# Optimization experiments

Hardware: AMD Instinct MI355X
Metric: run time of the kernel (lower is better)

Reference implementation:

```python
import jax, jax.numpy as jnp
import numpy as np
import math

B, SQ, SK, D = 32, 2048, 2048, 128


def setup_inputs() -> dict:
    key = jax.random.key(0)
    kq, kk, kv = jax.random.split(key, 3)
    queries = jax.random.normal(kq, (B, SQ, D), dtype=jnp.float32)
    keys = jax.random.normal(kk, (B, SK, D), dtype=jnp.float32)
    values = jax.random.normal(kv, (B, SK, D), dtype=jnp.float32)
    # causal mask: True = masked (future positions), broadcast over batch
    causal = jnp.triu(jnp.ones((SQ, SK), dtype=bool), k=1)
    mask = jnp.broadcast_to(causal, (B, SQ, SK))
    return {"queries": queries, "keys": keys, "values": values, "mask": mask}


def reference(queries, keys, values, mask):
    d = queries.shape[-1]
    scale = 1.0 / math.sqrt(d)
    # [B, Sq, Sk] score matrix (the module materializes this explicitly)
    scores = jnp.einsum("bqd,bkd->bqk", queries, keys) * scale
    scores = jnp.where(mask, -jnp.inf, scores)
    attn = jax.nn.softmax(scores, axis=-1)
    # dropout p=0.0 -> identity (eval parity)
    return jnp.einsum("bqk,bkd->bqd", attn, values)
```

## Files before the change

### kernel.cpp

```cpp
#include <hip/hip_runtime.h>
#include <hip/hip_bf16.h>

#define NB   32
#define SQL  2048
#define SKL  2048
#define DH   128
#define QBLK 128
#define KBLK 64

#define KSTR 136
#define VSTR 72
#define PSTR 72

typedef __attribute__((ext_vector_type(4))) float f32x4;
typedef __attribute__((ext_vector_type(8))) short s16x8;

__device__ __forceinline__ unsigned int pk2(float lo, float hi) {
  unsigned short a = __builtin_bit_cast(unsigned short, __float2bfloat16(lo));
  unsigned short b = __builtin_bit_cast(unsigned short, __float2bfloat16(hi));
  return (unsigned int)a | ((unsigned int)b << 16);
}

__global__ __launch_bounds__(512, 2)
void attn_fwd(const float* __restrict__ Qg, const float* __restrict__ Kg,
              const float* __restrict__ Vg, float* __restrict__ Og) {
  __shared__ __align__(16) unsigned short smem[2*64*KSTR + 2*128*VSTR + 8*16*PSTR];

  const int tid  = threadIdx.x;
  const int wid  = tid >> 6;
  const int lane = tid & 63;
  const int g    = lane >> 4;
  const int ln   = lane & 15;

  const int i    = blockIdx.x;
  const int half = i >> 8;
  const int idx  = i & 255;
  const int b    = idx >> 3;
  const int q3   = idx & 7;
  const int qt   = half ? q3 : (15 - q3);
  const int qb   = qt * QBLK;
  const int nt   = 2*qt + 2;

  const float* Qb = Qg + (size_t)b * SQL * DH;
  const float* Kb = Kg + (size_t)b * SKL * DH;
  const float* Vb = Vg + (size_t)b * SKL * DH;
  float* Ob = Og + (size_t)b * SQL * DH;

  const float qscale = 0.08838834764831845f * 1.4426950408889634f;

  s16x8 qf[4];
  {
    const float* qr = Qb + (size_t)(qb + 16*wid + ln) * DH + 8*g;
    #pragma unroll
    for (int c = 0; c < 4; ++c) {
      f32x4 a  = *(const f32x4*)(qr + 32*c);
      f32x4 b4 = *(const f32x4*)(qr + 32*c + 4);
      s16x8 q8;
      #pragma unroll
      for (int j = 0; j < 4; ++j) {
        q8[j]     = (short)(unsigned short)(pk2(a[j]  * qscale, 0.f) & 0xFFFF);
        q8[j + 4] = (short)(unsigned short)(pk2(b4[j] * qscale, 0.f) & 0xFFFF);
      }
      qf[c] = q8;
    }
  }

  f32x4 oacc[8];
  #pragma unroll
  for (int ot = 0; ot < 8; ++ot) oacc[ot] = (f32x4){0.f, 0.f, 0.f, 0.f};
  float m_run = -1e30f;
  float l_run = 0.f;

  const int qglob = qb + 16*wid + ln;
  const int qmax  = qb + 16*wid + 15;

  const int kcol  = tid & 31;
  const int krow0 = tid >> 5;
  const int vkq   = tid & 15;
  const int vdq   = tid >> 4;

  f32x4 kpre[4], vpre[4];

  {
    const float* ks = Kb;
    #pragma unroll
    for (int it = 0; it < 4; ++it)
      kpre[it] = *(const f32x4*)(ks + (size_t)(krow0 + 16*it) * DH + 4*kcol);
    const float* vs = Vb + 4*vdq;
    #pragma unroll
    for (int j = 0; j < 4; ++j)
      vpre[j] = *(const f32x4*)(vs + (size_t)(4*vkq + j) * DH);
  }

  for (int t = 0; t < nt; ++t) {
    const int buf = t & 1;
    const int kb  = t * KBLK;

    {
      unsigned short* Kl = smem + buf * (64*KSTR);
      #pragma unroll
      for (int it = 0; it < 4; ++it) {
        f32x4 v = kpre[it];
        uint2 pk = make_uint2(pk2(v[0], v[1]), pk2(v[2], v[3]));
        *(uint2*)&Kl[(krow0 + 16*it)*KSTR + 4*kcol] = pk;
      }
      unsigned short* Vl = smem + 2*(64*KSTR) + buf * (128*VSTR);
      #pragma unroll
      for (int j2 = 0; j2 < 4; ++j2) {
        uint2 pk = make_uint2(pk2(vpre[0][j2], vpre[1][j2]),
                              pk2(vpre[2][j2], vpre[3][j2]));
        *(uint2*)&Vl[(4*vdq + j2)*VSTR + 4*vkq] = pk;
      }
    }

    if (t + 1 < nt) {
      const int kn = (t + 1) * KBLK;
      const float* ks = Kb + (size_t)kn * DH;
      #pragma unroll
      for (int it = 0; it < 4; ++it)
        kpre[it] = *(const f32x4*)(ks + (size_t)(krow0 + 16*it) * DH + 4*kcol);
      const float* vs = Vb + (size_t)kn * DH + 4*vdq;
      #pragma unroll
      for (int j = 0; j < 4; ++j)
        vpre[j] = *(const f32x4*)(vs + (size_t)(4*vkq + j) * DH);
    }

    asm volatile("s_waitcnt lgkmcnt(0)" ::: "memory");
    __builtin_amdgcn_s_barrier();
    __builtin_amdgcn_sched_barrier(0);

    if (kb <= qmax) {
      const unsigned short* Kl = smem + buf * (64*KSTR);
      const unsigned short* Vl = smem + 2*(64*KSTR) + buf * (128*VSTR);
      unsigned short* Pl = smem + 2*(64*KSTR) + 2*(128*VSTR) + wid*(16*PSTR);

      f32x4 sacc[4];
      #pragma unroll
      for (int m = 0; m < 4; ++m) sacc[m] = (f32x4){0.f, 0.f, 0.f, 0.f};
      __builtin_amdgcn_s_setprio(1);
      #pragma unroll
      for (int c = 0; c < 4; ++c) {
        #pragma unroll
        for (int m = 0; m < 4; ++m) {
          s16x8 kf = *(const s16x8*)&Kl[(16*m + ln)*KSTR + 8*g + 32*c];
          sacc[m] = __builtin_amdgcn_mfma_f32_16x16x32_bf16(kf, qf[c], sacc[m], 0, 0, 0);
        }
      }
      __builtin_amdgcn_s_setprio(0);

      if (kb + KBLK - 1 > qb + 16*wid) {
        #pragma unroll
        for (int m = 0; m < 4; ++m)
          #pragma unroll
          for (int r = 0; r < 4; ++r) {
            const int kk = kb + 16*m + 4*g + r;
            if (kk > qglob) sacc[m][r] = -1e30f;
          }
      }

      float tmax = sacc[0][0];
      #pragma unroll
      for (int m = 0; m < 4; ++m)
        #pragma unroll
        for (int r = 0; r < 4; ++r) tmax = fmaxf(tmax, sacc[m][r]);
      tmax = fmaxf(tmax, __shfl_xor(tmax, 16));
      tmax = fmaxf(tmax, __shfl_xor(tmax, 32));
      const float mnew  = fmaxf(m_run, tmax);
      const float alpha = exp2f(m_run - mnew);
      float lsum = 0.f;
      unsigned int pw[4][2];
      #pragma unroll
      for (int m = 0; m < 4; ++m) {
        float p0 = exp2f(sacc[m][0] - mnew);
        float p1 = exp2f(sacc[m][1] - mnew);
        float p2 = exp2f(sacc[m][2] - mnew);
        float p3 = exp2f(sacc[m][3] - mnew);
        lsum += (p0 + p1) + (p2 + p3);
        pw[m][0] = pk2(p0, p1);
        pw[m][1] = pk2(p2, p3);
      }
      lsum += __shfl_xor(lsum, 16);
      lsum += __shfl_xor(lsum, 32);
      l_run = l_run * alpha + lsum;
      m_run = mnew;

      float ar[4];
      #pragma unroll
      for (int r = 0; r < 4; ++r) ar[r] = __shfl(alpha, 4*g + r);
      #pragma unroll
      for (int ot = 0; ot < 8; ++ot)
        #pragma unroll
        for (int r = 0; r < 4; ++r) oacc[ot][r] *= ar[r];

      {
        unsigned short* prow = Pl + ln*PSTR;
        #pragma unroll
        for (int m = 0; m < 4; ++m) {
          *(unsigned int*)&prow[16*m + 4*g]     = pw[m][0];
          *(unsigned int*)&prow[16*m + 4*g + 2] = pw[m][1];
        }
      }

      s16x8 pf[2];
      #pragma unroll
      for (int c2 = 0; c2 < 2; ++c2)
        pf[c2] = *(const s16x8*)&Pl[ln*PSTR + 8*g + 32*c2];
      __builtin_amdgcn_s_setprio(1);
      #pragma unroll
      for (int ot = 0; ot < 8; ++ot) {
        #pragma unroll
        for (int c2 = 0; c2 < 2; ++c2) {
          s16x8 vf = *(const s16x8*)&Vl[(16*ot + ln)*VSTR + 8*g + 32*c2];
          oacc[ot] = __builtin_amdgcn_mfma_f32_16x16x32_bf16(pf[c2], vf, oacc[ot], 0, 0, 0);
        }
      }
      __builtin_amdgcn_s_setprio(0);
    }
  }

  const float linv = 1.0f / l_run;
  float lr[4];
  #pragma unroll
  for (int r = 0; r < 4; ++r) lr[r] = __shfl(linv, 4*g + r);
  float* orow = Ob + (size_t)(qb + 16*wid) * DH + ln;
  #pragma unroll
  for (int ot = 0; ot < 8; ++ot)
    #pragma unroll
    for (int r = 0; r < 4; ++r)
      orow[(size_t)(4*g + r) * DH + 16*ot] = oacc[ot][r] * lr[r];
}

extern "C" void kernel_launch(void* const* d_in, const int* in_sizes, int n_in,
                              void* d_out, int out_size, void* d_ws, size_t ws_size,
                              hipStream_t stream) {
  const float* Q = (const float*)d_in[0];
  const float* K = (const float*)d_in[1];
  const float* V = (const float*)d_in[2];
  float* O = (float*)d_out;
  dim3 grid(NB * (SQL / QBLK));
  dim3 block(512);
  attn_fwd<<<grid, block, 0, stream>>>(Q, K, V, O);
}
```

Baseline: 103.6 us.

## Switch attention to 32x32 MFMA with 4 waves, swizzled LDS, register-resident P

Moves the kernel from 16x16x32 to 32x32x16 bf16 MFMA, with each of 4 waves now owning 32 query rows instead of 8 waves with 16 rows. The padded LDS strides are replaced by XOR-swizzled K/V tiles. P goes from registers into the PV MFMA through v_permlane32_swap rather than a round trip through LDS. The online softmax now skips the rescale unless the max grows by more than 8 (lazy rescaling), and packing uses v_cvt_pk_bf16. The aim is fewer LDS reads and writes, fewer instructions and fewer rescales per tile, at the cost of higher register pressure and fewer waves per block.

```diff
diff --git a/kernel.cpp b/kernel.cpp
--- a/kernel.cpp
+++ b/kernel.cpp
@@ -3,17 +3,21 @@
 
 #define NB   32
 #define SQL  2048
-#define SKL  2048
 #define DH   128
 #define QBLK 128
 #define KBLK 64
 
-#define KSTR 136
-#define VSTR 72
-#define PSTR 72
-
-typedef __attribute__((ext_vector_type(4))) float f32x4;
-typedef __attribute__((ext_vector_type(8))) short s16x8;
+typedef __attribute__((ext_vector_type(4)))  float f32x4;
+typedef __attribute__((ext_vector_type(16))) float f32x16;
+typedef __attribute__((ext_vector_type(8)))  short s16x8;
+typedef __attribute__((ext_vector_type(4)))  unsigned int u32x4;
+
+__device__ __forceinline__ unsigned int cvtpk_bf16(float lo, float hi) {
+  unsigned int r;
+  asm("v_cvt_pk_bf16_f32 %0, %1, %2" : "=v"(r) : "v"(lo), "v"(hi));
+  return r;
+}
+#define PLSWAP(x, y) asm volatile("v_permlane32_swap_b32 %0, %1" : "+v"(x), "+v"(y))
 
 __device__ __forceinline__ unsigned int pk2(float lo, float hi) {
   unsigned short a = __builtin_bit_cast(unsigned short, __float2bfloat16(lo));
@@ -21,16 +25,16 @@
   return (unsigned int)a | ((unsigned int)b << 16);
 }
 
-__global__ __launch_bounds__(512, 2)
+__global__ __launch_bounds__(256, 2)
 void attn_fwd(const float* __restrict__ Qg, const float* __restrict__ Kg,
               const float* __restrict__ Vg, float* __restrict__ Og) {
-  __shared__ __align__(16) unsigned short smem[2*64*KSTR + 2*128*VSTR + 8*16*PSTR];
+  __shared__ __align__(16) char smem[65536];
 
   const int tid  = threadIdx.x;
   const int wid  = tid >> 6;
   const int lane = tid & 63;
-  const int g    = lane >> 4;
-  const int ln   = lane & 15;
+  const int hi   = lane >> 5;
+  const int c    = lane & 31;
 
   const int i    = blockIdx.x;
   const int half = i >> 8;
@@ -39,195 +43,211 @@
   const int q3   = idx & 7;
   const int qt   = half ? q3 : (15 - q3);
   const int qb   = qt * QBLK;
-  const int nt   = 2*qt + 2;
+  const int nt   = 2 * qt + 2;
 
   const float* Qb = Qg + (size_t)b * SQL * DH;
-  const float* Kb = Kg + (size_t)b * SKL * DH;
-  const float* Vb = Vg + (size_t)b * SKL * DH;
+  const float* Kb = Kg + (size_t)b * SQL * DH;
+  const float* Vb = Vg + (size_t)b * SQL * DH;
   float* Ob = Og + (size_t)b * SQL * DH;
 
   const float qscale = 0.08838834764831845f * 1.4426950408889634f;
 
-  s16x8 qf[4];
+  s16x8 qf[8];
   {
-    const float* qr = Qb + (size_t)(qb + 16*wid + ln) * DH + 8*g;
-    #pragma unroll
-    for (int c = 0; c < 4; ++c) {
-      f32x4 a  = *(const f32x4*)(qr + 32*c);
-      f32x4 b4 = *(const f32x4*)(qr + 32*c + 4);
-      s16x8 q8;
-      #pragma unroll
-      for (int j = 0; j < 4; ++j) {
-        q8[j]     = (short)(unsigned short)(pk2(a[j]  * qscale, 0.f) & 0xFFFF);
-        q8[j + 4] = (short)(unsigned short)(pk2(b4[j] * qscale, 0.f) & 0xFFFF);
-      }
-      qf[c] = q8;
-    }
-  }
-
-  f32x4 oacc[8];
+    const float* qr = Qb + (size_t)(qb + 32*wid + c) * DH + 8*hi;
+    #pragma unroll
+    for (int ds = 0; ds < 8; ++ds) {
+      f32x4 a = *(const f32x4*)(qr + 16*ds);
+      f32x4 d = *(const f32x4*)(qr + 16*ds + 4);
+      u32x4 w;
+      w[0] = pk2(a[0]*qscale, a[1]*qscale);
+      w[1] = pk2(a[2]*qscale, a[3]*qscale);
+      w[2] = pk2(d[0]*qscale, d[1]*qscale);
+      w[3] = pk2(d[2]*qscale, d[3]*qscale);
+      qf[ds] = __builtin_bit_cast(s16x8, w);
+    }
+  }
+
+  f32x16 oacc[4];
   #pragma unroll
-  for (int ot = 0; ot < 8; ++ot) oacc[ot] = (f32x4){0.f, 0.f, 0.f, 0.f};
-  float m_run = -1e30f;
-  float l_run = 0.f;
-
-  const int qglob = qb + 16*wid + ln;
-  const int qmax  = qb + 16*wid + 15;
-
-  const int kcol  = tid & 31;
-  const int krow0 = tid >> 5;
-  const int vkq   = tid & 15;
-  const int vdq   = tid >> 4;
-
-  f32x4 kpre[4], vpre[4];
-
+  for (int nb = 0; nb < 4; ++nb) oacc[nb] = (f32x16){0.f};
+  float m_run = -1e30f, l_run = 0.f;
+
+  const int qglob = qb + 32*wid + c;
+  const int qhiw  = qb + 32*wid + 31;
+  const int qlow  = qb + 32*wid;
+
+  const int kr  = tid >> 4;
+  const int kc8 = tid & 15;
+  const int vkq = tid & 15;
+  const int vdq = tid >> 4;
+
+  f32x4 kpre[8], vpre[8];
   {
-    const float* ks = Kb;
-    #pragma unroll
-    for (int it = 0; it < 4; ++it)
-      kpre[it] = *(const f32x4*)(ks + (size_t)(krow0 + 16*it) * DH + 4*kcol);
-    const float* vs = Vb + 4*vdq;
-    #pragma unroll
-    for (int j = 0; j < 4; ++j)
-      vpre[j] = *(const f32x4*)(vs + (size_t)(4*vkq + j) * DH);
+    #pragma unroll
+    for (int it = 0; it < 4; ++it) {
+      const float* p = Kb + (size_t)(kr + 16*it) * DH + 8*kc8;
+      kpre[2*it]   = *(const f32x4*)(p);
+      kpre[2*it+1] = *(const f32x4*)(p + 4);
+    }
+    #pragma unroll
+    for (int dd = 0; dd < 2; ++dd)
+      #pragma unroll
+      for (int j = 0; j < 4; ++j)
+        vpre[4*dd + j] = *(const f32x4*)(Vb + (size_t)(4*vkq + j) * DH + 4*(vdq + 16*dd));
   }
 
   for (int t = 0; t < nt; ++t) {
     const int buf = t & 1;
     const int kb  = t * KBLK;
-
-    {
-      unsigned short* Kl = smem + buf * (64*KSTR);
-      #pragma unroll
-      for (int it = 0; it < 4; ++it) {
-        f32x4 v = kpre[it];
-        uint2 pk = make_uint2(pk2(v[0], v[1]), pk2(v[2], v[3]));
-        *(uint2*)&Kl[(krow0 + 16*it)*KSTR + 4*kcol] = pk;
-      }
-      unsigned short* Vl = smem + 2*(64*KSTR) + buf * (128*VSTR);
+    char* Kl = smem + buf * 16384;
+    char* Vl = smem + 32768 + buf * 16384;
+
+    #pragma unroll
+    for (int it = 0; it < 4; ++it) {
+      const int row = kr + 16*it;
+      f32x4 a = kpre[2*it], d2 = kpre[2*it+1];
+      u32x4 w;
+      w[0] = pk2(a[0], a[1]);  w[1] = pk2(a[2], a[3]);
+      w[2] = pk2(d2[0], d2[1]); w[3] = pk2(d2[2], d2[3]);
+      *(u32x4*)(Kl + ((row*256 + 16*kc8) ^ ((row & 7) << 4))) = w;
+    }
+    #pragma unroll
+    for (int dd = 0; dd < 2; ++dd)
       #pragma unroll
       for (int j2 = 0; j2 < 4; ++j2) {
-        uint2 pk = make_uint2(pk2(vpre[0][j2], vpre[1][j2]),
-                              pk2(vpre[2][j2], vpre[3][j2]));
-        *(uint2*)&Vl[(4*vdq + j2)*VSTR + 4*vkq] = pk;
-      }
-    }
+        const int row = 4*(vdq + 16*dd) + j2;
+        uint2 pkk = make_uint2(pk2(vpre[4*dd+0][j2], vpre[4*dd+1][j2]),
+                               pk2(vpre[4*dd+2][j2], vpre[4*dd+3][j2]));
+        *(uint2*)(Vl + ((row*128 + 8*vkq) ^ ((row & 7) << 4))) = pkk;
+      }
 
     if (t + 1 < nt) {
       const int kn = (t + 1) * KBLK;
       const float* ks = Kb + (size_t)kn * DH;
       #pragma unroll
-      for (int it = 0; it < 4; ++it)
-        kpre[it] = *(const f32x4*)(ks + (size_t)(krow0 + 16*it) * DH + 4*kcol);
-      const float* vs = Vb + (size_t)kn * DH + 4*vdq;
-      #pragma unroll
-      for (int j = 0; j < 4; ++j)
-        vpre[j] = *(const f32x4*)(vs + (size_t)(4*vkq + j) * DH);
+      for (int it = 0; it < 4; ++it) {
+        const float* p = ks + (size_t)(kr + 16*it) * DH + 8*kc8;
+        kpre[2*it]   = *(const f32x4*)(p);
+        kpre[2*it+1] = *(const f32x4*)(p + 4);
+      }
+      const float* vs = Vb + (size_t)kn * DH;
+      #pragma unroll
+      for (int dd = 0; dd < 2; ++dd)
+        #pragma unroll
+        for (int j = 0; j < 4; ++j)
+          vpre[4*dd + j] = *(const f32x4*)(vs + (size_t)(4*vkq + j) * DH + 4*(vdq + 16*dd));
     }
 
     asm volatile("s_waitcnt lgkmcnt(0)" ::: "memory");
     __builtin_amdgcn_s_barrier();
     __builtin_amdgcn_sched_barrier(0);
 
-    if (kb <= qmax) {
-      const unsigned short* Kl = smem + buf * (64*KSTR);
-      const unsigned short* Vl = smem + 2*(64*KSTR) + buf * (128*VSTR);
-      unsigned short* Pl = smem + 2*(64*KSTR) + 2*(128*VSTR) + wid*(16*PSTR);
-
-      f32x4 sacc[4];
-      #pragma unroll
-      for (int m = 0; m < 4; ++m) sacc[m] = (f32x4){0.f, 0.f, 0.f, 0.f};
+    if (kb <= qhiw) {
+      f32x16 sacc[2];
+      sacc[0] = (f32x16){0.f};
+      sacc[1] = (f32x16){0.f};
       __builtin_amdgcn_s_setprio(1);
       #pragma unroll
-      for (int c = 0; c < 4; ++c) {
-        #pragma unroll
-        for (int m = 0; m < 4; ++m) {
-          s16x8 kf = *(const s16x8*)&Kl[(16*m + ln)*KSTR + 8*g + 32*c];
-          sacc[m] = __builtin_amdgcn_mfma_f32_16x16x32_bf16(kf, qf[c], sacc[m], 0, 0, 0);
+      for (int ds = 0; ds < 8; ++ds) {
+        #pragma unroll
+        for (int mb = 0; mb < 2; ++mb) {
+          const int row = 32*mb + c;
+          s16x8 kf = *(const s16x8*)(Kl + ((row*256 + 32*ds + 16*hi) ^ ((c & 7) << 4)));
+          sacc[mb] = __builtin_amdgcn_mfma_f32_32x32x16_bf16(kf, qf[ds], sacc[mb], 0, 0, 0);
         }
       }
       __builtin_amdgcn_s_setprio(0);
 
-      if (kb + KBLK - 1 > qb + 16*wid) {
-        #pragma unroll
-        for (int m = 0; m < 4; ++m)
+      if (kb + KBLK - 1 > qlow) {
+        #pragma unroll
+        for (int mb = 0; mb < 2; ++mb)
           #pragma unroll
-          for (int r = 0; r < 4; ++r) {
-            const int kk = kb + 16*m + 4*g + r;
-            if (kk > qglob) sacc[m][r] = -1e30f;
+          for (int r = 0; r < 16; ++r) {
+            const int kk = kb + 32*mb + (r & 3) + 8*(r >> 2) + 4*hi;
+            if (kk > qglob) sacc[mb][r] = -1e30f;
           }
       }
 
-      float tmax = sacc[0][0];
-      #pragma unroll
-      for (int m = 0; m < 4; ++m)
-        #pragma unroll
-        for (int r = 0; r < 4; ++r) tmax = fmaxf(tmax, sacc[m][r]);
-      tmax = fmaxf(tmax, __shfl_xor(tmax, 16));
+      float mx[8];
+      #pragma unroll
+      for (int e = 0; e < 8; ++e)
+        mx[e] = fmaxf(fmaxf(sacc[0][e], sacc[0][e+8]), fmaxf(sacc[1][e], sacc[1][e+8]));
+      mx[0] = fmaxf(mx[0], mx[4]); mx[1] = fmaxf(mx[1], mx[5]);
+      mx[2] = fmaxf(mx[2], mx[6]); mx[3] = fmaxf(mx[3], mx[7]);
+      float tmax = fmaxf(fmaxf(mx[0], mx[1]), fmaxf(mx[2], mx[3]));
       tmax = fmaxf(tmax, __shfl_xor(tmax, 32));
-      const float mnew  = fmaxf(m_run, tmax);
-      const float alpha = exp2f(m_run - mnew);
+
+      if (!__all(tmax <= m_run + 8.0f)) {
+        const float mnew  = fmaxf(m_run, tmax);
+        const float alpha = exp2f(m_run - mnew);
+        #pragma unroll
+        for (int r = 0; r < 16; ++r) {
+          float av = __shfl(alpha, (r & 3) + 8*(r >> 2) + 4*hi);
+          #pragma unroll
+          for (int nb = 0; nb < 4; ++nb) oacc[nb][r] *= av;
+        }
+        l_run *= alpha;
+        m_run = mnew;
+      }
+
       float lsum = 0.f;
-      unsigned int pw[4][2];
-      #pragma unroll
-      for (int m = 0; m < 4; ++m) {
-        float p0 = exp2f(sacc[m][0] - mnew);
-        float p1 = exp2f(sacc[m][1] - mnew);
-        float p2 = exp2f(sacc[m][2] - mnew);
-        float p3 = exp2f(sacc[m][3] - mnew);
-        lsum += (p0 + p1) + (p2 + p3);
-        pw[m][0] = pk2(p0, p1);
-        pw[m][1] = pk2(p2, p3);
-      }
-      lsum += __shfl_xor(lsum, 16);
+      unsigned int u0[8], u1[8];
+      {
+        float p[16];
+        #pragma unroll
+        for (int r = 0; r < 16; ++r) p[r] = exp2f(sacc[0][r] - m_run);
+        lsum += ((p[0]+p[1])+(p[2]+p[3])) + ((p[4]+p[5])+(p[6]+p[7]))
+              + ((p[8]+p[9])+(p[10]+p[11])) + ((p[12]+p[13])+(p[14]+p[15]));
+        #pragma unroll
+        for (int w = 0; w < 8; ++w) u0[w] = cvtpk_bf16(p[2*w], p[2*w+1]);
+      }
+      {
+        float p[16];
+        #pragma unroll
+        for (int r = 0; r < 16; ++r) p[r] = exp2f(sacc[1][r] - m_run);
+        lsum += ((p[0]+p[1])+(p[2]+p[3])) + ((p[4]+p[5])+(p[6]+p[7]))
+              + ((p[8]+p[9])+(p[10]+p[11])) + ((p[12]+p[13])+(p[14]+p[15]));
+        #pragma unroll
+        for (int w = 0; w < 8; ++w) u1[w] = cvtpk_bf16(p[2*w], p[2*w+1]);
+      }
       lsum += __shfl_xor(lsum, 32);
-      l_run = l_run * alpha + lsum;
-      m_run = mnew;
-
-      float ar[4];
-      #pragma unroll
-      for (int r = 0; r < 4; ++r) ar[r] = __shfl(alpha, 4*g + r);
-      #pragma unroll
-      for (int ot = 0; ot < 8; ++ot)
-        #pragma unroll
-        for (int r = 0; r < 4; ++r) oacc[ot][r] *= ar[r];
-
-      {
-        unsigned short* prow = Pl + ln*PSTR;
-        #pragma unroll
-        for (int m = 0; m < 4; ++m) {
-          *(unsigned int*)&prow[16*m + 4*g]     = pw[m][0];
-          *(unsigned int*)&prow[16*m + 4*g + 2] = pw[m][1];
+      l_run += lsum;
+
+      PLSWAP(u0[0], u0[2]); PLSWAP(u0[1], u0[3]);
+      PLSWAP(u0[4], u0[6]); PLSWAP(u0[5], u0[7]);
+      PLSWAP(u1[0], u1[2]); PLSWAP(u1[1], u1[3]);
+      PLSWAP(u1[4], u1[6]); PLSWAP(u1[5], u1[7]);
+      s16x8 pa[4];
+      { u32x4 w = {u0[0], u0[1], u0[2], u0[3]}; pa[0] = __builtin_bit_cast(s16x8, w); }
+      { u32x4 w = {u0[4], u0[5], u0[6], u0[7]}; pa[1] = __builtin_bit_cast(s16x8, w); }
+      { u32x4 w = {u1[0], u1[1], u1[2], u1[3]}; pa[2] = __builtin_bit_cast(s16x8, w); }
+      { u32x4 w = {u1[4], u1[5], u1[6], u1[7]}; pa[3] = __builtin_bit_cast(s16x8, w); }
+
+      __builtin_amdgcn_s_setprio(1);
+      #pragma unroll
+      for (int nb = 0; nb < 4; ++nb) {
+        #pragma unroll
+        for (int ks = 0; ks < 4; ++ks) {
+          const int row = 32*nb + c;
+          s16x8 vf = *(const s16x8*)(Vl + ((row*128 + 32*ks + 16*hi) ^ ((c & 7) << 4)));
+          oacc[nb] = __builtin_amdgcn_mfma_f32_32x32x16_bf16(pa[ks], vf, oacc[nb], 0, 0, 0);
         }
       }
-
-      s16x8 pf[2];
-      #pragma unroll
-      for (int c2 = 0; c2 < 2; ++c2)
-        pf[c2] = *(const s16x8*)&Pl[ln*PSTR + 8*g + 32*c2];
-      __builtin_amdgcn_s_setprio(1);
-      #pragma unroll
-      for (int ot = 0; ot < 8; ++ot) {
-        #pragma unroll
-        for (int c2 = 0; c2 < 2; ++c2) {
-          s16x8 vf = *(const s16x8*)&Vl[(16*ot + ln)*VSTR + 8*g + 32*c2];
-          oacc[ot] = __builtin_amdgcn_mfma_f32_16x16x32_bf16(pf[c2], vf, oacc[ot], 0, 0, 0);
-        }
-      }
       __builtin_amdgcn_s_setprio(0);
     }
   }
 
   const float linv = 1.0f / l_run;
-  float lr[4];
+  float* Orow = Ob + (size_t)(qb + 32*wid) * DH;
   #pragma unroll
-  for (int r = 0; r < 4; ++r) lr[r] = __shfl(linv, 4*g + r);
-  float* orow = Ob + (size_t)(qb + 16*wid) * DH + ln;
-  #pragma unroll
-  for (int ot = 0; ot < 8; ++ot)
-    #pragma unroll
-    for (int r = 0; r < 4; ++r)
-      orow[(size_t)(4*g + r) * DH + 16*ot] = oacc[ot][r] * lr[r];
+  for (int r = 0; r < 16; ++r) {
+    const int q = (r & 3) + 8*(r >> 2) + 4*hi;
+    float lv = __shfl(linv, q);
+    #pragma unroll
+    for (int nb = 0; nb < 4; ++nb)
+      Orow[(size_t)q * DH + 32*nb + c] = oacc[nb][r] * lv;
+  }
 }
 
 extern "C" void kernel_launch(void* const* d_in, const int* in_sizes, int n_in,
@@ -238,6 +258,6 @@
   const float* V = (const float*)d_in[2];
   float* O = (float*)d_out;
   dim3 grid(NB * (SQL / QBLK));
-  dim3 block(512);
+  dim3 block(256);
   attn_fwd<<<grid, block, 0, stream>>>(Q, K, V, O);
 }
```

Measured after the change: 179.4 us. 73.3% more time.
